# Optimization experiments

Measured on AMD Instinct MI355X. Metric: run time of the kernel, lower is better.

The kernel has to match this reference:

```python
import jax, jax.numpy as jnp
import numpy as np

ALIGNED_H = 7
ALIGNED_W = 7
SPATIAL_SCALE = 0.0625  # 1/16


def setup_inputs() -> dict:
    key = jax.random.key(0)
    k1, k2, k3, k4, k5 = jax.random.split(key, 5)
    B, C, H, W = 4, 256, 100, 100
    K = 2048
    img = H / SPATIAL_SCALE  # 1600px image
    features = jax.random.normal(k1, (B, C, H, W), dtype=jnp.float32)
    batch_idx = jax.random.randint(k2, (K,), 0, B).astype(jnp.float32)
    x1 = jax.random.uniform(k3, (K,), minval=0.0, maxval=img - 200.0)
    y1 = jax.random.uniform(k4, (K,), minval=0.0, maxval=img - 200.0)
    wh = jax.random.uniform(k5, (K, 2), minval=32.0, maxval=200.0)
    rois = jnp.stack([batch_idx, x1, y1, x1 + wh[:, 0], y1 + wh[:, 1]], axis=1)
    return {"features": features, "rois": rois}


def _roi_align_dense(features, rois, Hs, Ws, scale):
    """Dense RoIAlign (crop_and_resize style): one bilinear sample per grid point.
    features: [B,C,H,W]; rois: [K,5] (batch_idx, x1,y1,x2,y2). Returns [K,C,Hs,Ws]."""
    B, C, H, W = features.shape
    feats = jnp.transpose(features, (0, 2, 3, 1))  # [B,H,W,C] for gather
    b = rois[:, 0].astype(jnp.int32)
    x1, y1, x2, y2 = (rois[:, i] * scale for i in (1, 2, 3, 4))
    ty = jnp.arange(Hs, dtype=features.dtype) / (Hs - 1)
    tx = jnp.arange(Ws, dtype=features.dtype) / (Ws - 1)
    ys = y1[:, None] + (y2 - y1)[:, None] * ty  # [K,Hs]
    xs = x1[:, None] + (x2 - x1)[:, None] * tx  # [K,Ws]

    y0 = jnp.floor(ys)
    x0 = jnp.floor(xs)
    wy = ys - y0  # [K,Hs]
    wx = xs - x0  # [K,Ws]
    y0i = jnp.clip(y0.astype(jnp.int32), 0, H - 1)
    y1i = jnp.clip(y0.astype(jnp.int32) + 1, 0, H - 1)
    x0i = jnp.clip(x0.astype(jnp.int32), 0, W - 1)
    x1i = jnp.clip(x0.astype(jnp.int32) + 1, 0, W - 1)

    bk = b[:, None, None]  # [K,1,1]

    def gather(yi, xi):  # yi: [K,Hs], xi: [K,Ws] -> [K,Hs,Ws,C]
        return feats[bk, yi[:, :, None], xi[:, None, :], :]

    wy_ = wy[:, :, None, None]  # [K,Hs,1,1]
    wx_ = wx[:, None, :, None]  # [K,1,Ws,1]
    v = (gather(y0i, x0i) * (1 - wy_) * (1 - wx_)
         + gather(y0i, x1i) * (1 - wy_) * wx_
         + gather(y1i, x0i) * wy_ * (1 - wx_)
         + gather(y1i, x1i) * wy_ * wx_)  # [K,Hs,Ws,C]
    return jnp.transpose(v, (0, 3, 1, 2))  # [K,C,Hs,Ws]


def _max_pool2d_3s2(x):
    return jax.lax.reduce_window(
        x, -jnp.inf, jax.lax.max,
        window_dimensions=(1, 1, 3, 3), window_strides=(1, 1, 2, 2),
        padding='VALID')


def reference(features, rois):
    dense = _roi_align_dense(features, rois, ALIGNED_H + 4, ALIGNED_W + 4, SPATIAL_SCALE)
    return _max_pool2d_3s2(dense)  # [K, C, 5, 5]
```

## Files before the change

kernel.cpp:

```cpp
#include <hip/hip_runtime.h>


constexpr int Bn = 4, Cn = 256, Hn = 100, Wn = 100;
constexpr int HWn = Hn * Wn;
constexpr int PAIRS = Cn / 2;
constexpr float SCALE = 0.0625f;

__device__ __forceinline__ unsigned int bfpack(float a, float b) {
    unsigned int ua = __float_as_uint(a), ub = __float_as_uint(b);
    ua = (ua + 0x7FFFu + ((ua >> 16) & 1u)) >> 16;
    ub = (ub + 0x7FFFu + ((ub >> 16) & 1u)) & 0xFFFF0000u;
    return ua | ub;
}
__device__ __forceinline__ float lo16(unsigned int u) { return __uint_as_float(u << 16); }
__device__ __forceinline__ float hi16(unsigned int u) { return __uint_as_float(u & 0xFFFF0000u); }

__global__ __launch_bounds__(256)
void nchw_to_nhwc_bf16(const float* __restrict__ in, unsigned int* __restrict__ out)
{
    __shared__ float tile[64][65];
    const int s0 = blockIdx.x * 64;
    const int c0 = blockIdx.y * 64;
    const int b  = blockIdx.z;
    const int t  = threadIdx.x;

    {
        const int cl = t >> 4;
        const int s4 = (t & 15) * 4;
        const float* ip = in + ((size_t)b * Cn + c0) * HWn + s0;
#pragma unroll
        for (int pass = 0; pass < 4; ++pass) {
            const int c = pass * 16 + cl;
            if (s0 + s4 + 3 < HWn) {
                const float4 v = *(const float4*)(ip + (size_t)c * HWn + s4);
                tile[c][s4 + 0] = v.x; tile[c][s4 + 1] = v.y;
                tile[c][s4 + 2] = v.z; tile[c][s4 + 3] = v.w;
            } else {
#pragma unroll
                for (int i = 0; i < 4; ++i)
                    tile[c][s4 + i] = (s0 + s4 + i < HWn) ? ip[(size_t)c * HWn + s4 + i] : 0.0f;
            }
        }
    }
    __syncthreads();
    {
        const int s = t >> 2;
        const int q = t & 3;
        if (s0 + s < HWn) {
            unsigned int* op = out + ((size_t)b * HWn + (s0 + s)) * PAIRS + (c0 >> 1);
#pragma unroll
            for (int i = 0; i < 4; ++i) {
                const int p = q * 2 + i * 8;
                uint2 v;
                v.x = bfpack(tile[2 * p + 0][s], tile[2 * p + 1][s]);
                v.y = bfpack(tile[2 * p + 2][s], tile[2 * p + 3][s]);
                *(uint2*)(op + p) = v;
            }
        }
    }
}

__global__ __launch_bounds__(128)
void roipool_pair(const unsigned int* __restrict__ f, const float* __restrict__ rois,
                  float* __restrict__ out)
{
    __shared__ float stage[2][PAIRS * 2 * 5 * 5 / 2];
    const int tid  = threadIdx.x;
    const int wid  = tid >> 6;
    const int lane = tid & 63;
    const int k    = blockIdx.x;

    const float x1 = rois[k * 5 + 1] * SCALE;
    const float y1 = rois[k * 5 + 2] * SCALE;
    const float x2 = rois[k * 5 + 3] * SCALE;
    const float y2 = rois[k * 5 + 4] * SCALE;
    const int   b  = __builtin_amdgcn_readfirstlane((int)rois[k * 5 + 0]);

    const int pi = wid * 64 + lane;
    const unsigned int* fb = f + (size_t)b * HWn * PAIRS;

    int   xo0[11], xo1[11];
    float wx[11];
#pragma unroll
    for (int j = 0; j < 11; ++j) {
        const float xs  = x1 + (x2 - x1) * ((float)j * 0.1f);
        const float x0f = floorf(xs);
        wx[j] = xs - x0f;
        const int x0i = (int)x0f;
        xo0[j] = __builtin_amdgcn_readfirstlane(min(max(x0i,     0), Wn - 1)) * PAIRS;
        xo1[j] = __builtin_amdgcn_readfirstlane(min(max(x0i + 1, 0), Wn - 1)) * PAIRS;
    }

    auto dorow = [&](int gy, float (&dlo)[5], float (&dhi)[5]) {
        const float ys  = y1 + (y2 - y1) * ((float)gy * 0.1f);
        const float y0f = floorf(ys);
        const float wy  = ys - y0f;
        const int   y0i = (int)y0f;
        const int r0 = __builtin_amdgcn_readfirstlane(min(max(y0i,     0), Hn - 1));
        const int r1 = __builtin_amdgcn_readfirstlane(min(max(y0i + 1, 0), Hn - 1));
        const unsigned int* rp0 = fb + (size_t)(r0 * Wn) * PAIRS;
        const unsigned int* rp1 = fb + (size_t)(r1 * Wn) * PAIRS;
#pragma unroll
        for (int j = 0; j < 11; ++j) {
            const unsigned int u00 = (rp0 + xo0[j])[pi];
            const unsigned int u01 = (rp0 + xo1[j])[pi];
            const unsigned int u10 = (rp1 + xo0[j])[pi];
            const unsigned int u11 = (rp1 + xo1[j])[pi];
            float a00 = lo16(u00), a01 = lo16(u01), a10 = lo16(u10), a11 = lo16(u11);
            float X0 = a00 + wx[j] * (a01 - a00);
            float X1 = a10 + wx[j] * (a11 - a10);
            const float sl = X0 + wy * (X1 - X0);
            float b00 = hi16(u00), b01 = hi16(u01), b10 = hi16(u10), b11 = hi16(u11);
            X0 = b00 + wx[j] * (b01 - b00);
            X1 = b10 + wx[j] * (b11 - b10);
            const float sh = X0 + wy * (X1 - X0);
            if (j == 0)      { dlo[0] = sl; dhi[0] = sh; }
            else if (j & 1)  { dlo[j >> 1] = fmaxf(dlo[j >> 1], sl);
                               dhi[j >> 1] = fmaxf(dhi[j >> 1], sh); }
            else {
                dlo[(j >> 1) - 1] = fmaxf(dlo[(j >> 1) - 1], sl);
                dhi[(j >> 1) - 1] = fmaxf(dhi[(j >> 1) - 1], sh);
                if (j < 10) { dlo[j >> 1] = sl; dhi[j >> 1] = sh; }
            }
        }
    };

    float plo[5], phi[5];
    dorow(0, plo, phi);
    float* stw = stage[wid];
    float* st0 = &stw[(2 * lane + 0) * 25];
    float* st1 = &stw[(2 * lane + 1) * 25];

#pragma unroll
    for (int ph = 0; ph < 5; ++ph) {
        float tlo[5], thi[5], nlo[5], nhi[5];
        dorow(2 * ph + 1, tlo, thi);
        dorow(2 * ph + 2, nlo, nhi);
#pragma unroll
        for (int pw = 0; pw < 5; ++pw) {
            st0[ph * 5 + pw] = fmaxf(fmaxf(plo[pw], tlo[pw]), nlo[pw]);
            st1[ph * 5 + pw] = fmaxf(fmaxf(phi[pw], thi[pw]), nhi[pw]);
            plo[pw] = nlo[pw]; phi[pw] = nhi[pw];
        }
    }

    asm volatile("" ::: "memory");

    float* ob = out + (size_t)k * (Cn * 25) + (size_t)wid * 3200;
#pragma unroll
    for (int i = 0; i < 25; ++i) {
        const int idx = (i * 64 + lane) * 2;
        *(float2*)(ob + idx) = *(const float2*)(stw + idx);
    }
}

__global__ __launch_bounds__(256)
void roialign_pool_fallback(const float* __restrict__ feats,
                            const float* __restrict__ rois,
                            float* __restrict__ out)
{
    __shared__ float smem[4][2][128];
    const int k    = blockIdx.x;
    const int tid  = threadIdx.x;
    const int wid  = tid >> 6;
    const int lane = tid & 63;

    const float x1 = rois[k * 5 + 1] * SCALE;
    const float y1 = rois[k * 5 + 2] * SCALE;
    const float x2 = rois[k * 5 + 3] * SCALE;
    const float y2 = rois[k * 5 + 4] * SCALE;
    const int   b  = (int)rois[k * 5 + 0];

    const int  p1   = 64 + lane;
    const bool act1 = (p1 < 121);
    int   o00[2], o01[2], o10[2], o11[2];
    float w00[2], w01[2], w10[2], w11[2];
#pragma unroll
    for (int r = 0; r < 2; ++r) {
        const int p  = (r == 0) ? lane : (act1 ? p1 : 120);
        const int gy = p / 11;
        const int gx = p - gy * 11;
        const float ys = y1 + (y2 - y1) * ((float)gy / 10.0f);
        const float xs = x1 + (x2 - x1) * ((float)gx / 10.0f);
        const float y0f = floorf(ys), x0f = floorf(xs);
        const float wy = ys - y0f, wxx = xs - x0f;
        const int y0i = (int)y0f, x0i = (int)x0f;
        const int y0c = min(max(y0i, 0), Hn - 1), y1c = min(max(y0i + 1, 0), Hn - 1);
        const int x0c = min(max(x0i, 0), Wn - 1), x1c = min(max(x0i + 1, 0), Wn - 1);
        o00[r] = y0c * Wn + x0c; o01[r] = y0c * Wn + x1c;
        o10[r] = y1c * Wn + x0c; o11[r] = y1c * Wn + x1c;
        w00[r] = (1.0f - wy) * (1.0f - wxx); w01[r] = (1.0f - wy) * wxx;
        w10[r] = wy * (1.0f - wxx);          w11[r] = wy * wxx;
    }
    const bool pool  = (lane < 25);
    const int  ph    = lane / 5;
    const int  pw    = lane - ph * 5;
    const int  pbase = (2 * ph) * 11 + 2 * pw;
    const float* base = feats + ((size_t)b * Cn + (size_t)wid * 64) * HWn;
    float*       op   = out + ((size_t)k * Cn + (size_t)wid * 64) * 25 + lane;
    for (int it = 0; it < 64; ++it) {
        const float* ff  = base + (size_t)it * HWn;
        float*       buf = smem[wid][it & 1];
        const float v0 = ff[o00[0]] * w00[0] + ff[o01[0]] * w01[0]
                       + ff[o10[0]] * w10[0] + ff[o11[0]] * w11[0];
        const float v1 = ff[o00[1]] * w00[1] + ff[o01[1]] * w01[1]
                       + ff[o10[1]] * w10[1] + ff[o11[1]] * w11[1];
        buf[lane] = v0;
        if (act1) buf[p1] = v1;
        if (pool) {
            float m =          buf[pbase +  0];
            m = fmaxf(m, buf[pbase +  1]);
            m = fmaxf(m, buf[pbase +  2]);
            m = fmaxf(m, buf[pbase + 11]);
            m = fmaxf(m, buf[pbase + 12]);
            m = fmaxf(m, buf[pbase + 13]);
            m = fmaxf(m, buf[pbase + 22]);
            m = fmaxf(m, buf[pbase + 23]);
            m = fmaxf(m, buf[pbase + 24]);
            op[it * 25] = m;
        }
    }
}

extern "C" void kernel_launch(void* const* d_in, const int* in_sizes, int n_in,
                              void* d_out, int out_size, void* d_ws, size_t ws_size,
                              hipStream_t stream) {
    const float* feats = (const float*)d_in[0];
    const float* rois  = (const float*)d_in[1];
    float*       out   = (float*)d_out;
    const int K = in_sizes[1] / 5;
    const size_t need = (size_t)Bn * HWn * PAIRS * sizeof(unsigned int);

    if (ws_size >= need) {
        unsigned int* nhwc = (unsigned int*)d_ws;
        dim3 tgrid((HWn + 63) / 64, Cn / 64, Bn);
        nchw_to_nhwc_bf16<<<tgrid, 256, 0, stream>>>(feats, nhwc);
        roipool_pair<<<K, 128, 0, stream>>>(nhwc, rois, out);
    } else {
        roialign_pool_fallback<<<K, 256, 0, stream>>>(feats, rois, out);
    }
}
```

Baseline: 51.44 us.

## Pair channels c and c+128 in bf16 packing and halve pool staging smem

```diff
diff --git a/kernel.cpp b/kernel.cpp
--- a/kernel.cpp
+++ b/kernel.cpp
@@ -20,25 +20,26 @@
 {
     __shared__ float tile[64][65];
     const int s0 = blockIdx.x * 64;
-    const int c0 = blockIdx.y * 64;
+    const int p0 = blockIdx.y * 32;
     const int b  = blockIdx.z;
     const int t  = threadIdx.x;
 
     {
         const int cl = t >> 4;
         const int s4 = (t & 15) * 4;
-        const float* ip = in + ((size_t)b * Cn + c0) * HWn + s0;
+        const float* ip = in + (size_t)b * Cn * HWn + s0;
 #pragma unroll
         for (int pass = 0; pass < 4; ++pass) {
-            const int c = pass * 16 + cl;
+            const int r  = pass * 16 + cl;
+            const int ch = (pass < 2) ? (p0 + r) : (p0 + 96 + r);
             if (s0 + s4 + 3 < HWn) {
-                const float4 v = *(const float4*)(ip + (size_t)c * HWn + s4);
-                tile[c][s4 + 0] = v.x; tile[c][s4 + 1] = v.y;
-                tile[c][s4 + 2] = v.z; tile[c][s4 + 3] = v.w;
+                const float4 v = *(const float4*)(ip + (size_t)ch * HWn + s4);
+                tile[r][s4 + 0] = v.x; tile[r][s4 + 1] = v.y;
+                tile[r][s4 + 2] = v.z; tile[r][s4 + 3] = v.w;
             } else {
 #pragma unroll
                 for (int i = 0; i < 4; ++i)
-                    tile[c][s4 + i] = (s0 + s4 + i < HWn) ? ip[(size_t)c * HWn + s4 + i] : 0.0f;
+                    tile[r][s4 + i] = (s0 + s4 + i < HWn) ? ip[(size_t)ch * HWn + s4 + i] : 0.0f;
             }
         }
     }
@@ -47,14 +48,14 @@
         const int s = t >> 2;
         const int q = t & 3;
         if (s0 + s < HWn) {
-            unsigned int* op = out + ((size_t)b * HWn + (s0 + s)) * PAIRS + (c0 >> 1);
+            unsigned int* op = out + ((size_t)b * HWn + (s0 + s)) * PAIRS + p0;
 #pragma unroll
             for (int i = 0; i < 4; ++i) {
-                const int p = q * 2 + i * 8;
+                const int li = q * 2 + i * 8;
                 uint2 v;
-                v.x = bfpack(tile[2 * p + 0][s], tile[2 * p + 1][s]);
-                v.y = bfpack(tile[2 * p + 2][s], tile[2 * p + 3][s]);
-                *(uint2*)(op + p) = v;
+                v.x = bfpack(tile[li    ][s], tile[li + 32][s]);
+                v.y = bfpack(tile[li + 1][s], tile[li + 33][s]);
+                *(uint2*)(op + li) = v;
             }
         }
     }
@@ -64,7 +65,7 @@
 void roipool_pair(const unsigned int* __restrict__ f, const float* __restrict__ rois,
                   float* __restrict__ out)
 {
-    __shared__ float stage[2][PAIRS * 2 * 5 * 5 / 2];
+    __shared__ float stage[2][1600];
     const int tid  = threadIdx.x;
     const int wid  = tid >> 6;
     const int lane = tid & 63;
@@ -125,11 +126,10 @@
         }
     };
 
-    float plo[5], phi[5];
+    float plo[5], phi[5], ohi[25];
     dorow(0, plo, phi);
     float* stw = stage[wid];
-    float* st0 = &stw[(2 * lane + 0) * 25];
-    float* st1 = &stw[(2 * lane + 1) * 25];
+    float* stl = &stw[lane * 25];
 
 #pragma unroll
     for (int ph = 0; ph < 5; ++ph) {
@@ -138,20 +138,27 @@
         dorow(2 * ph + 2, nlo, nhi);
 #pragma unroll
         for (int pw = 0; pw < 5; ++pw) {
-            st0[ph * 5 + pw] = fmaxf(fmaxf(plo[pw], tlo[pw]), nlo[pw]);
-            st1[ph * 5 + pw] = fmaxf(fmaxf(phi[pw], thi[pw]), nhi[pw]);
+            stl[ph * 5 + pw]  = fmaxf(fmaxf(plo[pw], tlo[pw]), nlo[pw]);
+            ohi[ph * 5 + pw]  = fmaxf(fmaxf(phi[pw], thi[pw]), nhi[pw]);
             plo[pw] = nlo[pw]; phi[pw] = nhi[pw];
         }
     }
 
     asm volatile("" ::: "memory");
-
-    float* ob = out + (size_t)k * (Cn * 25) + (size_t)wid * 3200;
-#pragma unroll
-    for (int i = 0; i < 25; ++i) {
-        const int idx = (i * 64 + lane) * 2;
-        *(float2*)(ob + idx) = *(const float2*)(stw + idx);
-    }
+    float* obl = out + (size_t)k * (Cn * 25) + (size_t)wid * 1600;
+#pragma unroll
+    for (int i = 0; i < 25; ++i)
+        obl[i * 64 + lane] = stw[i * 64 + lane];
+
+    asm volatile("" ::: "memory");
+#pragma unroll
+    for (int p = 0; p < 25; ++p)
+        stl[p] = ohi[p];
+    asm volatile("" ::: "memory");
+    float* obh = obl + 3200;
+#pragma unroll
+    for (int i = 0; i < 25; ++i)
+        obh[i * 64 + lane] = stw[i * 64 + lane];
 }
 
 __global__ __launch_bounds__(256)
@@ -233,7 +240,7 @@
 
     if (ws_size >= need) {
         unsigned int* nhwc = (unsigned int*)d_ws;
-        dim3 tgrid((HWn + 63) / 64, Cn / 64, Bn);
+        dim3 tgrid((HWn + 63) / 64, PAIRS / 32, Bn);
         nchw_to_nhwc_bf16<<<tgrid, 256, 0, stream>>>(feats, nhwc);
         roipool_pair<<<K, 128, 0, stream>>>(nhwc, rois, out);
     } else {
```

After: 45.57 us. 11.4% less time.
